# Kernel tuning notes

Hardware: AMD Instinct MI355X
Metric: run time of the kernel (lower is better)

Reference implementation:

```python
import jax, jax.numpy as jnp
import numpy as np

# Per-species MLP dims from CoefficientLayer._create_model (H, C, N, O), aev_dim=384
DIMS = {"h": [384, 160, 128, 96, 1], "c": [384, 144, 112, 96, 1], "n": [384, 128, 112, 96, 1], "o": [384, 128, 112, 96, 1]}


def setup_inputs() -> dict:
    key = jax.random.key(0)
    B, A, D = 256, 256, 384
    ks = jax.random.split(key, 64)
    inp = {}
    inp["species"] = jax.random.randint(ks[0], (B, A), 0, 4)  # species index 0..3
    inp["aev"] = jax.random.normal(ks[1], (B, A, D), dtype=jnp.float32)
    inp["b0"] = jnp.array([0.1, 0.2, 0.3, 0.4], dtype=jnp.float32)  # shifter intercepts
    inp["b1"] = jnp.array([1.0, 1.1, 0.9, 1.2], dtype=jnp.float32)  # shifter slopes
    ki = 2
    for name, dims in DIMS.items():
        for l in range(4):
            fi, fo = dims[l], dims[l + 1]
            inp[f"{name}w{l}"] = jax.random.normal(ks[ki], (fi, fo), dtype=jnp.float32) / np.float32(np.sqrt(fi))
            ki += 1
            inp[f"{name}b{l}"] = jnp.zeros((fo,), dtype=jnp.float32)
    return inp


def _mlp(x, ws, bs):
    # Linear -> CELU(0.1) x3 -> Linear(->1), squeeze last dim
    for i in range(3):
        x = jax.nn.celu(x @ ws[i] + bs[i], alpha=0.1)
    return (x @ ws[3] + bs[3])[..., 0]


def reference(species, aev, b0, b1,
              hw0, hb0, hw1, hb1, hw2, hb2, hw3, hb3,
              cw0, cb0, cw1, cb1, cw2, cb2, cw3, cb3,
              nw0, nb0, nw1, nb1, nw2, nb2, nw3, nb3,
              ow0, ob0, ow1, ob1, ow2, ob2, ow3, ob3):
    nets = [
        ([hw0, hw1, hw2, hw3], [hb0, hb1, hb2, hb3]),
        ([cw0, cw1, cw2, cw3], [cb0, cb1, cb2, cb3]),
        ([nw0, nw1, nw2, nw3], [nb0, nb1, nb2, nb3]),
        ([ow0, ow1, ow2, ow3], [ob0, ob1, ob2, ob3]),
    ]
    # ANIModel hard routing: each atom's coefficient comes from its species' network;
    # atoms with species == -1 (padding) stay 0.
    coef = jnp.zeros(species.shape, dtype=aev.dtype)
    for i, (ws, bs) in enumerate(nets):  # fixed small loop over 4 species
        coef = jnp.where(species == i, _mlp(aev, ws, bs), coef)
    # Shifter: result[mask_i] = b0[i] + b1[i] * coef[mask_i]; padding stays 0
    idx = jnp.clip(species, 0)
    return jnp.where(species >= 0, b0[idx] + b1[idx] * coef, jnp.zeros((), dtype=aev.dtype))
```

## Files before the change

### kernel.cpp

```cpp
#include <hip/hip_runtime.h>

typedef _Float16 f16;
typedef _Float16 f16x4 __attribute__((ext_vector_type(4)));
typedef _Float16 f16x8 __attribute__((ext_vector_type(8)));
typedef float f32x4 __attribute__((ext_vector_type(4)));
typedef unsigned short u16;
typedef unsigned int u32;

#define NATOMS 65536
#define CAP 17920

#define WS_LISTS_OFF 256
#define WS_W_OFF 524544
#define WS_W_ELEMS 350208
#define WS_ACT0_OFF (2u << 20)
#define WS_BIG (46u << 20)

#define BLK0 128
#define BLK12 64

#define ROWB 1536
#define TILEB (16 * ROWB)
#define FRAGS 24

struct ConvJob { const float* src; int K, N, KS, NT, CK, off; };

struct PrepParams {
  const int* species;
  int* counts;
  u16* lists;
  f16* wbase;
  ConvJob jobs[16];
};

struct GemmParams {
  const float* aev;
  const float* b0;
  const float* b1;
  const float* bias[4][4];
  const float* w3src[4];
  const f16* w[4][4];
  const int* counts;
  const u16* lists;
  f16* act0;
  float* out;
  int Nreal0[4];
  int Nreal1[4];
};

template <int N> struct AF { f16x8 v[N]; };

__global__ __launch_bounds__(256) void prep_kernel(PrepParams p) {
  int tid = threadIdx.x;
  if (blockIdx.x < 256) {
    __shared__ int wcnt[4][4];
    __shared__ int wbase[4][4];
    int i = blockIdx.x * 256 + tid;
    int s = p.species[i];
    int wave = tid >> 6, lane = tid & 63;
    unsigned long long m[4];
    #pragma unroll
    for (int t = 0; t < 4; t++) {
      m[t] = __ballot(s == t);
      if (lane == 0) wcnt[wave][t] = __popcll(m[t]);
    }
    __syncthreads();
    if (tid < 4) {
      int t = tid;
      int c0 = wcnt[0][t], c1 = wcnt[1][t], c2 = wcnt[2][t], c3 = wcnt[3][t];
      int base = atomicAdd(&p.counts[t], c0 + c1 + c2 + c3);
      wbase[0][t] = base;
      wbase[1][t] = base + c0;
      wbase[2][t] = base + c0 + c1;
      wbase[3][t] = base + c0 + c1 + c2;
    }
    __syncthreads();
    int rnk = __popcll(m[s] & ((1ull << lane) - 1ull));
    p.lists[s * NATOMS + wbase[wave][s] + rnk] = (u16)i;
  } else {
    int bx = blockIdx.x - 256;
    int job = bx / 30, bxin = bx - job * 30;
    ConvJob jb = p.jobs[job];
    int e = bxin * 256 + tid;
    int nslots = jb.KS * jb.NT * 64;
    if (e >= nslots) return;
    int frag = e >> 6, lane = e & 63;
    int c = frag / (jb.CK * jb.NT);
    int rem = frag - c * (jb.CK * jb.NT);
    int ckc = min(jb.CK, jb.KS - c * jb.CK);
    int nt = rem / ckc, ki = rem - nt * ckc;
    int ks = c * jb.CK + ki;
    int q = lane >> 4, nlo = lane & 15;
    int n = nt * 16 + nlo;
    int k0 = ks * 32 + q * 8;
    f16x8 v;
    #pragma unroll
    for (int j = 0; j < 8; j++) {
      int k = k0 + j;
      float x = (n < jb.N && k < jb.K) ? jb.src[k * jb.N + n] : 0.f;
      v[j] = (f16)x;
    }
    *(f16x8*)(p.wbase + jb.off + (size_t)e * 8) = v;
  }
}

__device__ __forceinline__ float celu01(float v) {
  return v > 0.f ? v : 0.1f * (__expf(v * 10.f) - 1.f);
}

__device__ __forceinline__ void stage_frag(const f16* g, f16* l, int lane) {
  __builtin_amdgcn_global_load_lds(
      (const __attribute__((address_space(1))) u32*)(g + lane * 8),
      (__attribute__((address_space(3))) u32*)l, 16, 0, 0);
}

__device__ __forceinline__ void dma16(const void* g, void* l) {
  __builtin_amdgcn_global_load_lds(
      (const __attribute__((address_space(1))) u32*)g,
      (__attribute__((address_space(3))) u32*)l, 16, 0, 0);
}

__device__ __forceinline__ void wait_vm(int n) {
  switch (n) {
    case 0: __builtin_amdgcn_s_waitcnt(0x0F70); break;
    case 1: __builtin_amdgcn_s_waitcnt(0x0F71); break;
    case 3: __builtin_amdgcn_s_waitcnt(0x0F73); break;
    case 4: __builtin_amdgcn_s_waitcnt(0x0F74); break;
    case 6: __builtin_amdgcn_s_waitcnt(0x0F76); break;
    default: __builtin_amdgcn_s_waitcnt(0x0F77); break;
  }
}

template <int NT0>
__device__ void k0_body(const GemmParams& p, int s, int bl, char* smem) {
  int tid = threadIdx.x, w = tid >> 6, lane = tid & 63;
  int q = lane >> 4, nlo = lane & 15;
  int cnt = min(p.counts[s], CAP);
  int ntiles = (cnt + 15) >> 4;
  int tpb = (ntiles + BLK0 - 1) / BLK0;
  int t0 = bl * tpb;
  int nt_blk = min(ntiles - t0, tpb);
  if (nt_blk <= 0) return;

  const u16* list = p.lists + s * NATOMS;
  u16* atoms_l = (u16*)(smem + 3 * TILEB);

  f16x8 wf[12];
  float bvv[4];
  if (w < NT0) {
    const f16* wg = p.w[s][0];
    #pragma unroll
    for (int ks = 0; ks < 12; ks++)
      wf[ks] = *(const f16x8*)(wg + (size_t)(ks * NT0 + w) * 512 + lane * 8);
    #pragma unroll
    for (int r = 0; r < 4; r++) {
      int n = w * 16 + q * 4 + r;
      bvv[r] = (n < p.Nreal0[s]) ? p.bias[s][0][n] : 0.f;
    }
  }
  f16* act = p.act0 + (size_t)s * CAP * 160;

  for (int idx = tid; idx < nt_blk * 16; idx += 640)
    atoms_l[idx] = list[min(t0 * 16 + idx, cnt - 1)];
  __syncthreads();

  auto stage = [&](int i) {
    char* buf = smem + (i % 3) * TILEB;
    #pragma unroll
    for (int j = 0; j < 3; j++) {
      int f = w * 3 + j;
      int o = f * 1024 + lane * 16;
      int row = o / ROWB;
      int intra = o - row * ROWB;
      int gin = intra ^ ((row & 7) << 4);
      int atom = atoms_l[i * 16 + row];
      dma16((const char*)p.aev + (size_t)atom * ROWB + gin, buf + f * 1024);
    }
  };

  if (w < 8) {
    stage(0);
    if (nt_blk > 1) stage(1);
    if (nt_blk > 2) stage(2);
  }

  for (int i = 0; i < nt_blk; i++) {
    if (w < 8) {
      int ahead = min(nt_blk - 1 - i, 2);
      wait_vm(3 * ahead + (i > 0 ? 1 : 0));
    }
    __builtin_amdgcn_s_barrier();
    asm volatile("" ::: "memory");
    if (w < NT0) {
      const char* buf = smem + (i % 3) * TILEB;
      int tb = (t0 + i) * 16;
      f32x4 acc = {0.f, 0.f, 0.f, 0.f};
      int base = nlo * ROWB + q * 32;
      int swz = (nlo & 7) << 4;
      #pragma unroll
      for (int ks = 0; ks < 12; ks++) {
        int lin = base + ks * 128;
        f32x4 u0 = *(const f32x4*)(buf + (lin ^ swz));
        f32x4 u1 = *(const f32x4*)(buf + ((lin + 16) ^ swz));
        f16x8 a = {(f16)u0[0], (f16)u0[1], (f16)u0[2], (f16)u0[3],
                   (f16)u1[0], (f16)u1[1], (f16)u1[2], (f16)u1[3]};
        acc = __builtin_amdgcn_mfma_f32_16x16x32_f16(wf[ks], a, acc, 0, 0, 0);
      }
      int row = tb + nlo;
      if (row < cnt) {
        f16x4 o;
        #pragma unroll
        for (int r = 0; r < 4; r++) o[r] = (f16)celu01(acc[r] + bvv[r]);
        *(f16x4*)(act + (size_t)row * 160 + w * 16 + q * 4) = o;
      }
    }
    asm volatile("" ::: "memory");
    __builtin_amdgcn_s_barrier();
    if (w < 8 && i + 3 < nt_blk) stage(i + 3);
  }
}

__global__ __launch_bounds__(640, 4) void k0_kernel(GemmParams p) {
  __shared__ __align__(16) char smem[3 * TILEB + 384];
  int s = blockIdx.x & 3, bl = blockIdx.x >> 2;
  switch (s) {
    case 0: k0_body<10>(p, 0, bl, smem); break;
    case 1: k0_body<10>(p, 1, bl, smem); break;
    case 2: k0_body<8>(p, 2, bl, smem); break;
    default: k0_body<8>(p, 3, bl, smem); break;
  }
}

template <int KS1>
__device__ void k12_body(const GemmParams& p, int s, int bl, f16* W1, f16* W2,
                         f16* T) {
  int tid = threadIdx.x, w = tid >> 6, lane = tid & 63;
  int q = lane >> 4, nlo = lane & 15;
  constexpr int NF1 = KS1 * 8;
  const f16* g1 = p.w[s][1];
  const f16* g2 = p.w[s][2];
  for (int f = w; f < NF1 + 24; f += 8) {
    if (f < NF1) stage_frag(g1 + (size_t)f * 512, W1 + f * 512, lane);
    else stage_frag(g2 + (size_t)(f - NF1) * 512, W2 + (f - NF1) * 512, lane);
  }
  int cnt = min(p.counts[s], CAP);
  int ntiles = (cnt + 15) >> 4;
  const u16* list = p.lists + s * NATOMS;
  int Nr1 = p.Nreal1[s];
  const float* bias1 = p.bias[s][1];
  const float* bias2 = p.bias[s][2];
  const float* w3 = p.w3src[s];
  float bv[8], b2v[6], w3v[6];
  #pragma unroll
  for (int nt = 0; nt < 8; nt++) {
    int n = nt * 16 + nlo;
    bv[nt] = (n < Nr1) ? bias1[n] : 0.f;
  }
  #pragma unroll
  for (int nt = 0; nt < 6; nt++) {
    int n = nt * 16 + nlo;
    b2v[nt] = bias2[n];
    w3v[nt] = w3[n];
  }
  float b3 = p.bias[s][3][0];
  float b0v = p.b0[s], b1v = p.b1[s];
  const f16* act0 = p.act0 + (size_t)s * CAP * 160;
  f16* Tw = T + (w * 16) * 160;
  __syncthreads();

  auto load_a1 = [&](int t) {
    AF<KS1> a;
    int ar = min(t * 16 + nlo, cnt - 1);
    const f16* ap = act0 + (size_t)ar * 160 + q * 8;
    #pragma unroll
    for (int ks = 0; ks < KS1; ks++)
      a.v[ks] = *(const f16x8*)(ap + ks * 32);
    return a;
  };

  int t = bl * 8 + w;
  if (t >= ntiles) return;
  AF<KS1> a1 = load_a1(t);
  while (true) {
    int tn = t + BLK12 * 8;
    AF<KS1> a1n;
    if (tn < ntiles) a1n = load_a1(tn);
    int tb = t * 16;
    f32x4 acc1[8];
    #pragma unroll
    for (int nt = 0; nt < 8; nt++) acc1[nt] = f32x4{0.f, 0.f, 0.f, 0.f};
    #pragma unroll
    for (int ks = 0; ks < KS1; ks++) {
      #pragma unroll
      for (int nt = 0; nt < 8; nt++) {
        f16x8 b = *(const f16x8*)(W1 + (ks * 8 + nt) * 512 + lane * 8);
        acc1[nt] = __builtin_amdgcn_mfma_f32_16x16x32_f16(a1.v[ks], b, acc1[nt], 0, 0, 0);
      }
    }
    #pragma unroll
    for (int nt = 0; nt < 8; nt++) {
      #pragma unroll
      for (int r = 0; r < 4; r++)
        Tw[(q * 4 + r) * 160 + nt * 16 + nlo] = (f16)celu01(acc1[nt][r] + bv[nt]);
    }
    AF<4> a2;
    #pragma unroll
    for (int ks = 0; ks < 4; ks++)
      a2.v[ks] = *(const f16x8*)(Tw + nlo * 160 + ks * 32 + q * 8);
    f32x4 acc2[6];
    #pragma unroll
    for (int nt = 0; nt < 6; nt++) acc2[nt] = f32x4{0.f, 0.f, 0.f, 0.f};
    #pragma unroll
    for (int ks = 0; ks < 4; ks++) {
      #pragma unroll
      for (int nt = 0; nt < 6; nt++) {
        f16x8 b = *(const f16x8*)(W2 + (ks * 6 + nt) * 512 + lane * 8);
        acc2[nt] = __builtin_amdgcn_mfma_f32_16x16x32_f16(a2.v[ks], b, acc2[nt], 0, 0, 0);
      }
    }
    float pr[4] = {0.f, 0.f, 0.f, 0.f};
    #pragma unroll
    for (int nt = 0; nt < 6; nt++) {
      #pragma unroll
      for (int r = 0; r < 4; r++) {
        float v = celu01(acc2[nt][r] + b2v[nt]);
        pr[r] += v * w3v[nt];
      }
    }
    #pragma unroll
    for (int m = 1; m < 16; m <<= 1) {
      #pragma unroll
      for (int r = 0; r < 4; r++) pr[r] += __shfl_xor(pr[r], m);
    }
    if (nlo == 0) {
      #pragma unroll
      for (int r = 0; r < 4; r++) {
        int row = tb + q * 4 + r;
        if (row < cnt) p.out[list[row]] = b0v + b1v * (pr[r] + b3);
      }
    }
    if (tn >= ntiles) break;
    a1 = a1n;
    t = tn;
  }
}

__global__ __launch_bounds__(512, 2) void k12_kernel(GemmParams p) {
  __shared__ __align__(16) f16 W1[5 * 8 * 512];
  __shared__ __align__(16) f16 W2[4 * 6 * 512];
  __shared__ __align__(16) f16 T[8 * 16 * 160];
  int s = blockIdx.x & 3, bl = blockIdx.x >> 2;
  switch (s) {
    case 0: k12_body<5>(p, 0, bl, W1, W2, T); break;
    case 1: k12_body<5>(p, 1, bl, W1, W2, T); break;
    case 2: k12_body<4>(p, 2, bl, W1, W2, T); break;
    default: k12_body<4>(p, 3, bl, W1, W2, T); break;
  }
}


extern "C" void kernel_launch(void* const* d_in, const int* in_sizes, int n_in,
                              void* d_out, int out_size, void* d_ws, size_t ws_size,
                              hipStream_t stream) {
  if (ws_size < WS_BIG) return;

  const int* species = (const int*)d_in[0];
  const float* aev = (const float*)d_in[1];
  const float* b0 = (const float*)d_in[2];
  const float* b1 = (const float*)d_in[3];

  static const int F1[4]  = {160, 144, 128, 128};
  static const int F1p[4] = {160, 160, 128, 128};
  static const int F2[4]  = {128, 112, 112, 112};

  char* wsb = (char*)d_ws;
  int* counts = (int*)wsb;
  u16* lists = (u16*)(wsb + WS_LISTS_OFF);
  f16* wbase = (f16*)(wsb + WS_W_OFF);

  PrepParams pp;
  pp.species = species; pp.counts = counts; pp.lists = lists; pp.wbase = wbase;

  GemmParams mp;
  mp.aev = aev; mp.b0 = b0; mp.b1 = b1;
  mp.counts = counts; mp.lists = lists; mp.out = (float*)d_out;
  mp.act0 = (f16*)(wsb + WS_ACT0_OFF);

  int off = 0, ji = 0;
  for (int s = 0; s < 4; s++) {
    int K[4]  = {384, F1[s], F2[s], 96};
    int N[4]  = {F1[s], F2[s], 96, 1};
    int KS[4] = {12, F1p[s] / 32, 4, 3};
    int NT[4] = {F1p[s] / 16, 8, 6, 1};
    int CK[4] = {1, 1, 1, 3};
    for (int l = 0; l < 4; l++) {
      const float* w = (const float*)d_in[4 + s * 8 + l * 2];
      const float* b = (const float*)d_in[4 + s * 8 + l * 2 + 1];
      pp.jobs[ji].src = w;
      pp.jobs[ji].K = K[l];
      pp.jobs[ji].N = N[l];
      pp.jobs[ji].KS = KS[l];
      pp.jobs[ji].NT = NT[l];
      pp.jobs[ji].CK = CK[l];
      pp.jobs[ji].off = off;
      mp.w[s][l] = wbase + off;
      mp.bias[s][l] = b;
      off += KS[l] * NT[l] * 512;
      ji++;
    }
    mp.w3src[s] = (const float*)d_in[4 + s * 8 + 6];
    mp.Nreal0[s] = F1[s];
    mp.Nreal1[s] = F2[s];
  }

  hipMemsetAsync(d_ws, 0, 64, stream);
  prep_kernel<<<dim3(256 + 480), 256, 0, stream>>>(pp);
  k0_kernel<<<dim3(4 * BLK0), 640, 0, stream>>>(mp);
  k12_kernel<<<dim3(4 * BLK12), 512, 0, stream>>>(mp);
}
```

Before: 257.5 us.

## Stage AEV tiles through registers as fp16 with double-buffered LDS

The first-layer GEMM kernel no longer uses direct global-to-LDS DMA of fp32 AEV rows into a triple buffer. Stager waves now load fp32 into registers, convert to fp16, and write a swizzled half-size tile into a double-buffered LDS region, with the next tile's global load issued one iteration ahead. This halves LDS footprint and LDS read traffic and removes the per-MFMA fp32-to-fp16 conversion in compute waves, allowing higher occupancy (launch bound raised to 5). The cost is register pressure from in-flight loads and conversion work on the stager waves, plus shallower prefetch depth.

Result: no change. 260.3 us (+1.1%).

```diff
diff --git a/kernel.cpp b/kernel.cpp
--- a/kernel.cpp
+++ b/kernel.cpp
@@ -20,8 +20,8 @@
 #define BLK12 64
 
 #define ROWB 1536
-#define TILEB (16 * ROWB)
-#define FRAGS 24
+#define ROWH 768
+#define TILEH 12288
 
 struct ConvJob { const float* src; int K, N, KS, NT, CK, off; };
 
@@ -114,23 +114,6 @@
       (__attribute__((address_space(3))) u32*)l, 16, 0, 0);
 }
 
-__device__ __forceinline__ void dma16(const void* g, void* l) {
-  __builtin_amdgcn_global_load_lds(
-      (const __attribute__((address_space(1))) u32*)g,
-      (__attribute__((address_space(3))) u32*)l, 16, 0, 0);
-}
-
-__device__ __forceinline__ void wait_vm(int n) {
-  switch (n) {
-    case 0: __builtin_amdgcn_s_waitcnt(0x0F70); break;
-    case 1: __builtin_amdgcn_s_waitcnt(0x0F71); break;
-    case 3: __builtin_amdgcn_s_waitcnt(0x0F73); break;
-    case 4: __builtin_amdgcn_s_waitcnt(0x0F74); break;
-    case 6: __builtin_amdgcn_s_waitcnt(0x0F76); break;
-    default: __builtin_amdgcn_s_waitcnt(0x0F77); break;
-  }
-}
-
 template <int NT0>
 __device__ void k0_body(const GemmParams& p, int s, int bl, char* smem) {
   int tid = threadIdx.x, w = tid >> 6, lane = tid & 63;
@@ -143,7 +126,7 @@
   if (nt_blk <= 0) return;
 
   const u16* list = p.lists + s * NATOMS;
-  u16* atoms_l = (u16*)(smem + 3 * TILEB);
+  u16* atoms_l = (u16*)(smem + 2 * TILEH);
 
   f16x8 wf[12];
   float bvv[4];
@@ -164,49 +147,58 @@
     atoms_l[idx] = list[min(t0 * 16 + idx, cnt - 1)];
   __syncthreads();
 
-  auto stage = [&](int i) {
-    char* buf = smem + (i % 3) * TILEB;
+  bool stager = (w < 8);
+  int frow[3], fintra[3];
+  #pragma unroll
+  for (int j = 0; j < 3; j++) {
+    int o32 = (w + 8 * j) * 1024 + lane * 16;
+    frow[j] = o32 / ROWB;
+    fintra[j] = o32 - frow[j] * ROWB;
+  }
+
+  f32x4 ld[3];
+  auto issue = [&](int i) {
     #pragma unroll
     for (int j = 0; j < 3; j++) {
-      int f = w * 3 + j;
-      int o = f * 1024 + lane * 16;
-      int row = o / ROWB;
-      int intra = o - row * ROWB;
-      int gin = intra ^ ((row & 7) << 4);
-      int atom = atoms_l[i * 16 + row];
-      dma16((const char*)p.aev + (size_t)atom * ROWB + gin, buf + f * 1024);
+      int atom = atoms_l[i * 16 + frow[j]];
+      ld[j] = *(const f32x4*)((const char*)p.aev + (size_t)atom * ROWB + fintra[j]);
     }
   };
-
-  if (w < 8) {
-    stage(0);
-    if (nt_blk > 1) stage(1);
-    if (nt_blk > 2) stage(2);
-  }
+  auto write_lds = [&](int i) {
+    char* buf = smem + (i & 1) * TILEH;
+    #pragma unroll
+    for (int j = 0; j < 3; j++) {
+      int o16 = (w + 8 * j) * 512 + lane * 8;
+      int addr = o16 ^ ((frow[j] & 7) << 4);
+      f16x4 h = {(f16)ld[j][0], (f16)ld[j][1], (f16)ld[j][2], (f16)ld[j][3]};
+      *(f16x4*)(buf + addr) = h;
+    }
+  };
+
+  if (stager) {
+    issue(0);
+    write_lds(0);
+    if (nt_blk > 1) issue(1);
+  }
+  asm volatile("s_waitcnt lgkmcnt(0)" ::: "memory");
+  __builtin_amdgcn_s_barrier();
 
   for (int i = 0; i < nt_blk; i++) {
-    if (w < 8) {
-      int ahead = min(nt_blk - 1 - i, 2);
-      wait_vm(3 * ahead + (i > 0 ? 1 : 0));
-    }
-    __builtin_amdgcn_s_barrier();
-    asm volatile("" ::: "memory");
+    if (stager) {
+      if (i + 1 < nt_blk) write_lds(i + 1);
+      if (i + 2 < nt_blk) issue(i + 2);
+    }
     if (w < NT0) {
-      const char* buf = smem + (i % 3) * TILEB;
-      int tb = (t0 + i) * 16;
+      const char* buf = smem + (i & 1) * TILEH;
+      int swz = (nlo & 7) << 4;
+      int base = nlo * ROWH + q * 16;
       f32x4 acc = {0.f, 0.f, 0.f, 0.f};
-      int base = nlo * ROWB + q * 32;
-      int swz = (nlo & 7) << 4;
       #pragma unroll
       for (int ks = 0; ks < 12; ks++) {
-        int lin = base + ks * 128;
-        f32x4 u0 = *(const f32x4*)(buf + (lin ^ swz));
-        f32x4 u1 = *(const f32x4*)(buf + ((lin + 16) ^ swz));
-        f16x8 a = {(f16)u0[0], (f16)u0[1], (f16)u0[2], (f16)u0[3],
-                   (f16)u1[0], (f16)u1[1], (f16)u1[2], (f16)u1[3]};
+        f16x8 a = *(const f16x8*)(buf + ((base + ks * 64) ^ swz));
         acc = __builtin_amdgcn_mfma_f32_16x16x32_f16(wf[ks], a, acc, 0, 0, 0);
       }
-      int row = tb + nlo;
+      int row = (t0 + i) * 16 + nlo;
       if (row < cnt) {
         f16x4 o;
         #pragma unroll
@@ -214,14 +206,13 @@
         *(f16x4*)(act + (size_t)row * 160 + w * 16 + q * 4) = o;
       }
     }
-    asm volatile("" ::: "memory");
+    asm volatile("s_waitcnt lgkmcnt(0)" ::: "memory");
     __builtin_amdgcn_s_barrier();
-    if (w < 8 && i + 3 < nt_blk) stage(i + 3);
-  }
-}
-
-__global__ __launch_bounds__(640, 4) void k0_kernel(GemmParams p) {
-  __shared__ __align__(16) char smem[3 * TILEB + 384];
+  }
+}
+
+__global__ __launch_bounds__(640, 5) void k0_kernel(GemmParams p) {
+  __shared__ __align__(16) char smem[2 * TILEH + 384];
   int s = blockIdx.x & 3, bl = blockIdx.x >> 2;
   switch (s) {
     case 0: k0_body<10>(p, 0, bl, smem); break;
```
